# Performance work log

Hardware: AMD Instinct MI355X
Metric: run time of the kernel (lower is better)

The kernel has to match this reference:

```python
import jax, jax.numpy as jnp
import numpy as np

N = 50000      # nodes
E = 400000     # edges (before self-loops)
DIN = 128
HID = 128
HEADS = 4
DOUT = 64
NEG_SLOPE = 0.2  # PyG GATConv default


def setup_inputs() -> dict:
    key = jax.random.key(0)
    ks = jax.random.split(key, 14)

    def w(k, shape, fan_in):
        return jax.random.normal(k, shape, dtype=jnp.float32) * (1.0 / np.sqrt(fan_in))

    x = jax.random.normal(ks[0], (N, DIN), dtype=jnp.float32)
    edge_index = jax.random.randint(ks[1], (2, E), 0, N, dtype=jnp.int32)

    # layer 1: DIN -> HEADS*HID (concat)
    W1 = w(ks[2], (DIN, HEADS * HID), DIN)
    a_src1 = w(ks[3], (HEADS, HID), HID)
    a_dst1 = w(ks[4], (HEADS, HID), HID)
    b1 = jnp.zeros((HEADS * HID,), jnp.float32)
    # layer 2: HEADS*HID -> HEADS*HID (concat)
    W2 = w(ks[5], (HEADS * HID, HEADS * HID), HEADS * HID)
    a_src2 = w(ks[6], (HEADS, HID), HID)
    a_dst2 = w(ks[7], (HEADS, HID), HID)
    b2 = jnp.zeros((HEADS * HID,), jnp.float32)
    # layer 3: HEADS*HID -> DOUT, heads=1, concat=False (mean)
    W3 = w(ks[8], (HEADS * HID, DOUT), HEADS * HID)
    a_src3 = w(ks[9], (1, DOUT), DOUT)
    a_dst3 = w(ks[10], (1, DOUT), DOUT)
    b3 = jnp.zeros((DOUT,), jnp.float32)

    return dict(x=x, edge_index=edge_index,
                W1=W1, a_src1=a_src1, a_dst1=a_dst1, b1=b1,
                W2=W2, a_src2=a_src2, a_dst2=a_dst2, b2=b2,
                W3=W3, a_src3=a_src3, a_dst3=a_dst3, b3=b3)


def _gat_layer(x, src, dst, W, a_src, a_dst, n):
    """One GATConv (eval mode, self-loops already in src/dst). Returns [n, H, C]."""
    H, C = a_src.shape
    h = (x @ W).reshape(n, H, C)                        # projected features
    alpha_s = jnp.einsum('nhc,hc->nh', h, a_src)        # per-node src logits
    alpha_d = jnp.einsum('nhc,hc->nh', h, a_dst)
    e = jax.nn.leaky_relu(alpha_s[src] + alpha_d[dst], NEG_SLOPE)  # [E', H]
    # segment softmax over incoming edges of each dst node
    m = jax.ops.segment_max(e, dst, num_segments=n)
    e = jnp.exp(e - m[dst])
    s = jax.ops.segment_sum(e, dst, num_segments=n)
    alpha = e / (s[dst] + 1e-16)                        # [E', H]
    msg = h[src] * alpha[:, :, None]                    # [E', H, C]
    return jax.ops.segment_sum(msg, dst, num_segments=n)


def reference(x, edge_index, W1, a_src1, a_dst1, b1,
              W2, a_src2, a_dst2, b2, W3, a_src3, a_dst3, b3):
    n = x.shape[0]
    loops = jnp.arange(n, dtype=edge_index.dtype)       # PyG add_self_loops=True
    src = jnp.concatenate([edge_index[0], loops])
    dst = jnp.concatenate([edge_index[1], loops])

    h = _gat_layer(x, src, dst, W1, a_src1, a_dst1, n).reshape(n, -1) + b1
    h = jax.nn.elu(h)   # dropout is identity in eval mode
    h = _gat_layer(h, src, dst, W2, a_src2, a_dst2, n).reshape(n, -1) + b2
    h = jax.nn.elu(h)
    out = _gat_layer(h, src, dst, W3, a_src3, a_dst3, n)[:, 0, :] + b3  # heads=1, concat=False
    return out
```

## Files before the change

kernel.cpp:

```cpp
#include <hip/hip_runtime.h>
#include <hip/hip_bf16.h>


typedef __attribute__((ext_vector_type(8))) short bf16x8;
typedef __attribute__((ext_vector_type(4))) float f32x4;

__device__ __forceinline__ float bflo(unsigned w) { return __uint_as_float(w << 16); }
__device__ __forceinline__ float bfhi(unsigned w) { return __uint_as_float(w & 0xffff0000u); }
__device__ __forceinline__ float leaky(float x) { return x > 0.f ? x : 0.2f * x; }


__global__ void k_count(const int* __restrict__ ei, int E, int N, int* __restrict__ cnt) {
    int e = blockIdx.x * blockDim.x + threadIdx.x;
    int tot = E + N;
    if (e >= tot) return;
    int d = (e < E) ? ei[E + e] : (e - E);
    atomicAdd(&cnt[d], 1);
}

__global__ void k_scan1(const int* __restrict__ cnt, int N, int* __restrict__ rp,
                        int* __restrict__ blksum) {
    __shared__ int sdata[256];
    int t = threadIdx.x;
    int base = blockIdx.x * 1024;
    int v[4];
    int loc = 0;
#pragma unroll
    for (int i = 0; i < 4; i++) {
        int idx = base + t * 4 + i;
        v[i] = (idx < N) ? ((cnt[idx] + 3) & ~3) : 0;
        loc += v[i];
    }
    int x = loc;
    sdata[t] = x;
    __syncthreads();
    for (int off = 1; off < 256; off <<= 1) {
        int y = (t >= off) ? sdata[t - off] : 0;
        __syncthreads();
        x += y;
        sdata[t] = x;
        __syncthreads();
    }
    int run = x - loc;
#pragma unroll
    for (int i = 0; i < 4; i++) {
        int idx = base + t * 4 + i;
        if (idx < N) rp[idx] = run;
        run += v[i];
    }
    if (t == 255) blksum[blockIdx.x] = x;
}

__global__ void k_scan2(const int* __restrict__ blksum, int nblk, int* __restrict__ blkoff) {
    int l = threadIdx.x;
    int v = (l < nblk) ? blksum[l] : 0;
    int x = v;
#pragma unroll
    for (int off = 1; off < 64; off <<= 1) {
        int y = __shfl_up(x, off);
        if (l >= off) x += y;
    }
    if (l < nblk) blkoff[l] = x - v;
}

__global__ void k_scan3(int* __restrict__ rp, const int* __restrict__ blkoff,
                        const int* __restrict__ blksum, int N, int nblk,
                        int* __restrict__ cur) {
    int i = blockIdx.x * blockDim.x + threadIdx.x;
    if (i < N) {
        int v = rp[i] + blkoff[i >> 10];
        rp[i] = v;
        cur[i] = v;
    }
    if (i == 0) rp[N] = blkoff[nblk - 1] + blksum[nblk - 1];
}

__global__ void k_fill(const int* __restrict__ ei, int E, int N, int* __restrict__ cur,
                       int* __restrict__ col, int* __restrict__ dste) {
    int e = blockIdx.x * blockDim.x + threadIdx.x;
    int tot = E + N;
    if (e >= tot) return;
    int s, d;
    if (e < E) { s = ei[e]; d = ei[E + e]; }
    else       { s = e - E; d = e - E; }
    int p = atomicAdd(&cur[d], 1);
    col[p] = s;
    dste[p] = d;
}

__global__ void k_padfill(const int* __restrict__ rp, const int* __restrict__ cnt, int N,
                          int* __restrict__ col, int* __restrict__ dste) {
    int n = blockIdx.x * blockDim.x + threadIdx.x;
    if (n >= N) return;
    int p = rp[n] + cnt[n];
    int end = rp[n + 1];
    for (; p < end; p++) {
        col[p] = 0;
        dste[p] = -1;
    }
}


__global__ void k_cast_pad(const float* __restrict__ X, __hip_bfloat16* __restrict__ Xb,
                           int n_elems, int total) {
    int i = (blockIdx.x * blockDim.x + threadIdx.x) * 4;
    if (i >= total) return;
    float4 v = make_float4(0.f, 0.f, 0.f, 0.f);
    if (i < n_elems) v = *(const float4*)&X[i];
    __hip_bfloat16 tmp[4] = {__float2bfloat16(v.x), __float2bfloat16(v.y),
                             __float2bfloat16(v.z), __float2bfloat16(v.w)};
    *(ushort4*)&Xb[i] = *(const ushort4*)tmp;
}

__global__ void k_castT(const float* __restrict__ W, __hip_bfloat16* __restrict__ Wt,
                        int K, int Nw) {
    __shared__ float t[32][33];
    int k0 = blockIdx.x * 32, n0 = blockIdx.y * 32;
    int tx = threadIdx.x & 31, ty = threadIdx.x >> 5;
    for (int i = ty; i < 32; i += 8) t[i][tx] = W[(size_t)(k0 + i) * Nw + n0 + tx];
    __syncthreads();
    for (int i = ty; i < 32; i += 8)
        Wt[(size_t)(n0 + i) * K + k0 + tx] = __float2bfloat16(t[tx][i]);
}


template <int BN>
__global__ void __launch_bounds__(256) k_gemm_mfma(const __hip_bfloat16* __restrict__ A,
                                                   const __hip_bfloat16* __restrict__ Bt,
                                                   __hip_bfloat16* __restrict__ C,
                                                   int M, int Nn, int K) {
    constexpr int BM = 128, BK = 64;
    constexpr int WM = 64;
    constexpr int WN = BN / 2;
    constexpr int MREP = WM / 16;
    constexpr int NREP = WN / 16;

    __shared__ __hip_bfloat16 lds[(BM + BN) * BK];
    __hip_bfloat16* As = lds;
    __hip_bfloat16* Bs = lds + BM * BK;

    const int tid = threadIdx.x;
    const int wave = tid >> 6;
    const int lane = tid & 63;
    const int wm0 = (wave >> 1) * WM;
    const int wn0 = (wave & 1) * WN;
    const int m0 = blockIdx.y * BM;
    const int n0 = blockIdx.x * BN;
    const int fr = lane & 15;
    const int fq = lane >> 4;

    f32x4 acc[MREP][NREP] = {};

    for (int kt = 0; kt < K; kt += BK) {
        const __hip_bfloat16* srcA = A + (size_t)m0 * K + kt;
#pragma unroll
        for (int it = 0; it < BM * 8 / 256; ++it) {
            int gb = it * 256 + wave * 64;
            int g = gb + lane;
            int row = g >> 3;
            int kg = (g & 7) ^ (row & 7);
            const __hip_bfloat16* gsrc = srcA + (size_t)row * K + kg * 8;
            __builtin_amdgcn_global_load_lds(
                (const __attribute__((address_space(1))) void*)gsrc,
                (__attribute__((address_space(3))) void*)(As + gb * 8), 16, 0, 0);
        }
        const __hip_bfloat16* srcB = Bt + (size_t)n0 * K + kt;
#pragma unroll
        for (int it = 0; it < BN * 8 / 256; ++it) {
            int gb = it * 256 + wave * 64;
            int g = gb + lane;
            int row = g >> 3;
            int kg = (g & 7) ^ (row & 7);
            const __hip_bfloat16* gsrc = srcB + (size_t)row * K + kg * 8;
            __builtin_amdgcn_global_load_lds(
                (const __attribute__((address_space(1))) void*)gsrc,
                (__attribute__((address_space(3))) void*)(Bs + gb * 8), 16, 0, 0);
        }
        __syncthreads();

#pragma unroll
        for (int sl = 0; sl < 2; ++sl) {
            int ke = sl * 32 + fq * 8;
            bf16x8 af[MREP], bfr[NREP];
#pragma unroll
            for (int i = 0; i < MREP; ++i) {
                int row = wm0 + i * 16 + fr;
                int e = (row * BK + ke) ^ ((row & 7) << 3);
                af[i] = *(const bf16x8*)(As + e);
            }
#pragma unroll
            for (int j = 0; j < NREP; ++j) {
                int row = wn0 + j * 16 + fr;
                int e = (row * BK + ke) ^ ((row & 7) << 3);
                bfr[j] = *(const bf16x8*)(Bs + e);
            }
#pragma unroll
            for (int i = 0; i < MREP; ++i)
#pragma unroll
                for (int j = 0; j < NREP; ++j)
                    acc[i][j] = __builtin_amdgcn_mfma_f32_16x16x32_bf16(
                        af[i], bfr[j], acc[i][j], 0, 0, 0);
        }
        __syncthreads();
    }

#pragma unroll
    for (int i = 0; i < MREP; ++i) {
#pragma unroll
        for (int j = 0; j < NREP; ++j) {
            int col = n0 + wn0 + j * 16 + fr;
#pragma unroll
            for (int r = 0; r < 4; ++r) {
                int rowg = m0 + wm0 + i * 16 + fq * 4 + r;
                C[(size_t)rowg * Nn + col] = __float2bfloat16(acc[i][j][r]);
            }
        }
    }
}


template <int C, int H>
__global__ void k_alpha(const __hip_bfloat16* __restrict__ h, const float* __restrict__ a_src,
                        const float* __restrict__ a_dst, float* __restrict__ as_out,
                        float* __restrict__ ad_out, int N) {
    int w = (blockIdx.x * blockDim.x + threadIdx.x) >> 6;
    int lane = threadIdx.x & 63;
    int n = w / H, hd = w % H;
    if (n >= N) return;
    const __hip_bfloat16* hp = h + (size_t)n * (C * H) + hd * C;
    const float* asp = a_src + hd * C;
    const float* adp = a_dst + hd * C;
    float s1 = 0.f, s2 = 0.f;
    if constexpr (C == 128) {
        unsigned wrd = *(const unsigned*)(hp + 2 * lane);
        float f0 = bflo(wrd), f1 = bfhi(wrd);
        float2 a2 = *(const float2*)(asp + 2 * lane);
        float2 d2 = *(const float2*)(adp + 2 * lane);
        s1 = f0 * a2.x + f1 * a2.y;
        s2 = f0 * d2.x + f1 * d2.y;
    } else {
        float v = __bfloat162float(hp[lane & 63]);
        s1 = v * asp[lane];
        s2 = v * adp[lane];
    }
#pragma unroll
    for (int off = 32; off >= 1; off >>= 1) {
        s1 += __shfl_xor(s1, off);
        s2 += __shfl_xor(s2, off);
    }
    if (lane == 0) {
        as_out[n * H + hd] = s1;
        ad_out[n * H + hd] = s2;
    }
}


__global__ void k_edgew4(const int* __restrict__ col, const int* __restrict__ dste,
                         const float* __restrict__ as, const float* __restrict__ ad,
                         float* __restrict__ wbuf, const int* __restrict__ rp, int N, int EP) {
    int e = blockIdx.x * blockDim.x + threadIdx.x;
    int rpN = rp[N];
    if (e >= rpN) return;
    int d = dste[e];
    if (d < 0) {
        wbuf[e] = 0.f;
        wbuf[EP + e] = 0.f;
        wbuf[2 * EP + e] = 0.f;
        wbuf[3 * EP + e] = 0.f;
        return;
    }
    int s = col[e];
    float4 a = *(const float4*)&as[s * 4];
    float4 b = *(const float4*)&ad[d * 4];
    wbuf[e]          = __expf(leaky(a.x + b.x));
    wbuf[EP + e]     = __expf(leaky(a.y + b.y));
    wbuf[2 * EP + e] = __expf(leaky(a.z + b.z));
    wbuf[3 * EP + e] = __expf(leaky(a.w + b.w));
}

__global__ void k_edgew1(const int* __restrict__ col, const int* __restrict__ dste,
                         const float* __restrict__ as, const float* __restrict__ ad,
                         float* __restrict__ wbuf, const int* __restrict__ rp, int N) {
    int e = blockIdx.x * blockDim.x + threadIdx.x;
    int rpN = rp[N];
    if (e >= rpN) return;
    int d = dste[e];
    if (d < 0) { wbuf[e] = 0.f; return; }
    wbuf[e] = __expf(leaky(as[col[e]] + ad[d]));
}


template <bool DO_ELU>
__global__ void k_gather512(const __hip_bfloat16* __restrict__ hfeat,
                            const float* __restrict__ wbuf, const int* __restrict__ rp,
                            const int* __restrict__ col, const float* __restrict__ bias,
                            __hip_bfloat16* __restrict__ out, int N, int EP) {
    int w = (blockIdx.x * blockDim.x + threadIdx.x) >> 6;
    int lane = threadIdx.x & 63;
    if (w >= N) return;
    int d = w;
    int r0 = rp[d], r1 = rp[d + 1];
    const float* wp = wbuf + (size_t)(lane >> 4) * EP;

    float acc[8] = {};
    float wsum = 0.f;
    for (int e = r0; e < r1; e += 4) {
        int4 c4 = *(const int4*)&col[e];
        float4 w4 = *(const float4*)&wp[e];
        uint4 v0 = *(const uint4*)(hfeat + (size_t)c4.x * 512 + lane * 8);
        uint4 v1 = *(const uint4*)(hfeat + (size_t)c4.y * 512 + lane * 8);
        uint4 v2 = *(const uint4*)(hfeat + (size_t)c4.z * 512 + lane * 8);
        uint4 v3 = *(const uint4*)(hfeat + (size_t)c4.w * 512 + lane * 8);
        wsum += (w4.x + w4.y) + (w4.z + w4.w);
        acc[0] += w4.x * bflo(v0.x); acc[1] += w4.x * bfhi(v0.x);
        acc[2] += w4.x * bflo(v0.y); acc[3] += w4.x * bfhi(v0.y);
        acc[4] += w4.x * bflo(v0.z); acc[5] += w4.x * bfhi(v0.z);
        acc[6] += w4.x * bflo(v0.w); acc[7] += w4.x * bfhi(v0.w);
        acc[0] += w4.y * bflo(v1.x); acc[1] += w4.y * bfhi(v1.x);
        acc[2] += w4.y * bflo(v1.y); acc[3] += w4.y * bfhi(v1.y);
        acc[4] += w4.y * bflo(v1.z); acc[5] += w4.y * bfhi(v1.z);
        acc[6] += w4.y * bflo(v1.w); acc[7] += w4.y * bfhi(v1.w);
        acc[0] += w4.z * bflo(v2.x); acc[1] += w4.z * bfhi(v2.x);
        acc[2] += w4.z * bflo(v2.y); acc[3] += w4.z * bfhi(v2.y);
        acc[4] += w4.z * bflo(v2.z); acc[5] += w4.z * bfhi(v2.z);
        acc[6] += w4.z * bflo(v2.w); acc[7] += w4.z * bfhi(v2.w);
        acc[0] += w4.w * bflo(v3.x); acc[1] += w4.w * bfhi(v3.x);
        acc[2] += w4.w * bflo(v3.y); acc[3] += w4.w * bfhi(v3.y);
        acc[4] += w4.w * bflo(v3.z); acc[5] += w4.w * bfhi(v3.z);
        acc[6] += w4.w * bflo(v3.w); acc[7] += w4.w * bfhi(v3.w);
    }

    float inv = 1.0f / (wsum + 1e-16f);
    __hip_bfloat16 tmp[8];
#pragma unroll
    for (int j = 0; j < 8; j++) {
        float v = acc[j] * inv + bias[lane * 8 + j];
        if (DO_ELU) v = v > 0.f ? v : expm1f(v);
        tmp[j] = __float2bfloat16(v);
    }
    *(float4*)(out + (size_t)d * 512 + lane * 8) = *(const float4*)tmp;
}


__global__ void k_gather64(const __hip_bfloat16* __restrict__ hfeat,
                           const float* __restrict__ wbuf, const int* __restrict__ rp,
                           const int* __restrict__ col, const float* __restrict__ bias,
                           float* __restrict__ out, int N) {
    int w = (blockIdx.x * blockDim.x + threadIdx.x) >> 6;
    int lane = threadIdx.x & 63;
    if (w >= N) return;
    int d = w;
    int r0 = rp[d], r1 = rp[d + 1];
    int g = lane >> 4, cl = lane & 15;

    float a0 = 0.f, a1 = 0.f, a2 = 0.f, a3 = 0.f, wsum = 0.f;
    for (int e0 = r0; e0 < r1; e0 += 4) {
        int e = e0 + g;
        int s = col[e];
        float wf = wbuf[e];
        uint2 q = *(const uint2*)(hfeat + (size_t)s * 64 + cl * 4);
        wsum += wf;
        a0 += wf * bflo(q.x);
        a1 += wf * bfhi(q.x);
        a2 += wf * bflo(q.y);
        a3 += wf * bfhi(q.y);
    }
#pragma unroll
    for (int off = 16; off <= 32; off <<= 1) {
        a0 += __shfl_xor(a0, off);
        a1 += __shfl_xor(a1, off);
        a2 += __shfl_xor(a2, off);
        a3 += __shfl_xor(a3, off);
        wsum += __shfl_xor(wsum, off);
    }
    if (g == 0) {
        float inv = 1.0f / (wsum + 1e-16f);
        float4 b4 = *(const float4*)&bias[cl * 4];
        float4 o = make_float4(a0 * inv + b4.x, a1 * inv + b4.y,
                               a2 * inv + b4.z, a3 * inv + b4.w);
        *(float4*)(out + (size_t)d * 64 + cl * 4) = o;
    }
}


extern "C" void kernel_launch(void* const* d_in, const int* in_sizes, int n_in,
                              void* d_out, int out_size, void* d_ws, size_t ws_size,
                              hipStream_t stream) {
    const float* x   = (const float*)d_in[0];
    const int*   ei  = (const int*)d_in[1];
    const float* W1  = (const float*)d_in[2];
    const float* as1 = (const float*)d_in[3];
    const float* ad1 = (const float*)d_in[4];
    const float* b1  = (const float*)d_in[5];
    const float* W2  = (const float*)d_in[6];
    const float* as2 = (const float*)d_in[7];
    const float* ad2 = (const float*)d_in[8];
    const float* b2  = (const float*)d_in[9];
    const float* W3  = (const float*)d_in[10];
    const float* as3 = (const float*)d_in[11];
    const float* ad3 = (const float*)d_in[12];
    const float* b3  = (const float*)d_in[13];

    const int N = in_sizes[0] / 128;
    const int E = in_sizes[1] / 2;
    const int Etot = E + N;
    const int EP = (Etot + 3 * N + 255) & ~255;
    const int Mp = (N + 127) & ~127;

    char* ws = (char*)d_ws;
    size_t off = 0;
    auto alloc = [&](size_t bytes) -> void* {
        void* p = ws + off;
        off = (off + bytes + 255) & ~(size_t)255;
        return p;
    };
    __hip_bfloat16* hbuf = (__hip_bfloat16*)alloc((size_t)Mp * 512 * 2);
    __hip_bfloat16* fbuf = (__hip_bfloat16*)alloc((size_t)Mp * 512 * 2);
    __hip_bfloat16* xb   = (__hip_bfloat16*)alloc((size_t)Mp * 128 * 2);
    __hip_bfloat16* Wt1  = (__hip_bfloat16*)alloc((size_t)512 * 128 * 2);
    __hip_bfloat16* Wt2  = (__hip_bfloat16*)alloc((size_t)512 * 512 * 2);
    __hip_bfloat16* Wt3  = (__hip_bfloat16*)alloc((size_t)64 * 512 * 2);
    float* aS   = (float*)alloc((size_t)N * 4 * 4);
    float* aD   = (float*)alloc((size_t)N * 4 * 4);
    float* wbuf = (float*)alloc((size_t)EP * 4 * 4);
    int* cnt  = (int*)alloc((size_t)N * 4);
    int* rp   = (int*)alloc((size_t)(N + 1) * 4);
    int* cur  = (int*)alloc((size_t)N * 4);
    int* col  = (int*)alloc((size_t)EP * 4);
    int* dste = (int*)alloc((size_t)EP * 4);
    int* blks = (int*)alloc(64 * 4);
    int* blko = (int*)alloc(64 * 4);

    hipMemsetAsync(cnt, 0, (size_t)N * 4, stream);
    int thr = 256;
    k_count<<<(Etot + thr - 1) / thr, thr, 0, stream>>>(ei, E, N, cnt);
    int nblk = (N + 1023) / 1024;
    k_scan1<<<nblk, 256, 0, stream>>>(cnt, N, rp, blks);
    k_scan2<<<1, 64, 0, stream>>>(blks, nblk, blko);
    k_scan3<<<(N + 255) / 256, 256, 0, stream>>>(rp, blko, blks, N, nblk, cur);
    k_fill<<<(Etot + thr - 1) / thr, thr, 0, stream>>>(ei, E, N, cur, col, dste);
    k_padfill<<<(N + 255) / 256, 256, 0, stream>>>(rp, cnt, N, col, dste);

    {
        int total = Mp * 128;
        k_cast_pad<<<(total / 4 + 255) / 256, 256, 0, stream>>>(x, xb, N * 128, total);
        dim3 g1(128 / 32, 512 / 32);
        k_castT<<<g1, 256, 0, stream>>>(W1, Wt1, 128, 512);
        dim3 g2(512 / 32, 512 / 32);
        k_castT<<<g2, 256, 0, stream>>>(W2, Wt2, 512, 512);
        dim3 g3(512 / 32, 64 / 32);
        k_castT<<<g3, 256, 0, stream>>>(W3, Wt3, 512, 64);
    }

    int alphaBlocks4 = (int)(((size_t)N * 4 * 64 + 255) / 256);
    int alphaBlocks1 = (int)(((size_t)N * 64 + 255) / 256);
    int edgeBlocks = (EP + 255) / 256;
    int gatBlocks = (N + 3) / 4;
    dim3 gemmG(512 / 128, Mp / 128);
    dim3 gemmG3(1, Mp / 128);

    k_gemm_mfma<128><<<gemmG, 256, 0, stream>>>(xb, Wt1, hbuf, Mp, 512, 128);
    k_alpha<128, 4><<<alphaBlocks4, 256, 0, stream>>>(hbuf, as1, ad1, aS, aD, N);
    k_edgew4<<<edgeBlocks, 256, 0, stream>>>(col, dste, aS, aD, wbuf, rp, N, EP);
    k_gather512<true><<<gatBlocks, 256, 0, stream>>>(hbuf, wbuf, rp, col, b1, fbuf, N, EP);

    k_gemm_mfma<128><<<gemmG, 256, 0, stream>>>(fbuf, Wt2, hbuf, Mp, 512, 512);
    k_alpha<128, 4><<<alphaBlocks4, 256, 0, stream>>>(hbuf, as2, ad2, aS, aD, N);
    k_edgew4<<<edgeBlocks, 256, 0, stream>>>(col, dste, aS, aD, wbuf, rp, N, EP);
    k_gather512<true><<<gatBlocks, 256, 0, stream>>>(hbuf, wbuf, rp, col, b2, fbuf, N, EP);

    k_gemm_mfma<64><<<gemmG3, 256, 0, stream>>>(fbuf, Wt3, hbuf, Mp, 64, 512);
    k_alpha<64, 1><<<alphaBlocks1, 256, 0, stream>>>(hbuf, as3, ad3, aS, aD, N);
    k_edgew1<<<edgeBlocks, 256, 0, stream>>>(col, dste, aS, aD, wbuf, rp, N);
    k_gather64<<<gatBlocks, 256, 0, stream>>>(hbuf, wbuf, rp, col, b3, (float*)d_out, N);
}
```

Measured before the change: 437.6 us.

## Reorder layer-1 GAT to aggregate raw inputs before projection, fuse bias+ELU into GEMM

Layer 1 now computes attention logits directly from the bf16 inputs using the precomputed products W1·a_src and W1·a_dst. It aggregates the 128-wide inputs per head before the projection, then runs a per-head batched GEMM with bias and ELU fused into the epilogue. This replaces a 512-wide gather over projected features with a 128-wide gather per head. The layer-2 gather is split across heads via grid z, and the padding fill is folded into the scan kernel, which removes one launch. The cost is an extra aggregated buffer and a GEMM over four 128-column blocks, and the reordering changes where bf16 rounding occurs.

```diff
diff --git a/kernel.cpp b/kernel.cpp
--- a/kernel.cpp
+++ b/kernel.cpp
@@ -8,6 +8,11 @@
 __device__ __forceinline__ float bflo(unsigned w) { return __uint_as_float(w << 16); }
 __device__ __forceinline__ float bfhi(unsigned w) { return __uint_as_float(w & 0xffff0000u); }
 __device__ __forceinline__ float leaky(float x) { return x > 0.f ? x : 0.2f * x; }
+__device__ __forceinline__ unsigned pack2(float a, float b) {
+    unsigned ua = __bfloat16_as_ushort(__float2bfloat16(a));
+    unsigned ub = __bfloat16_as_ushort(__float2bfloat16(b));
+    return ua | (ub << 16);
+}
 
 
 __global__ void k_count(const int* __restrict__ ei, int E, int N, int* __restrict__ cnt) {
@@ -64,13 +69,20 @@
 }
 
 __global__ void k_scan3(int* __restrict__ rp, const int* __restrict__ blkoff,
-                        const int* __restrict__ blksum, int N, int nblk,
-                        int* __restrict__ cur) {
+                        const int* __restrict__ blksum, const int* __restrict__ cnt,
+                        int N, int nblk, int* __restrict__ cur,
+                        int* __restrict__ col, int* __restrict__ dste) {
     int i = blockIdx.x * blockDim.x + threadIdx.x;
     if (i < N) {
         int v = rp[i] + blkoff[i >> 10];
         rp[i] = v;
         cur[i] = v;
+        int c = cnt[i];
+        int pad = ((c + 3) & ~3) - c;
+        for (int p = 0; p < pad; p++) {
+            col[v + c + p] = 0;
+            dste[v + c + p] = -1;
+        }
     }
     if (i == 0) rp[N] = blkoff[nblk - 1] + blksum[nblk - 1];
 }
@@ -88,18 +100,6 @@
     dste[p] = d;
 }
 
-__global__ void k_padfill(const int* __restrict__ rp, const int* __restrict__ cnt, int N,
-                          int* __restrict__ col, int* __restrict__ dste) {
-    int n = blockIdx.x * blockDim.x + threadIdx.x;
-    if (n >= N) return;
-    int p = rp[n] + cnt[n];
-    int end = rp[n + 1];
-    for (; p < end; p++) {
-        col[p] = 0;
-        dste[p] = -1;
-    }
-}
-
 
 __global__ void k_cast_pad(const float* __restrict__ X, __hip_bfloat16* __restrict__ Xb,
                            int n_elems, int total) {
@@ -123,12 +123,63 @@
         Wt[(size_t)(n0 + i) * K + k0 + tx] = __float2bfloat16(t[tx][i]);
 }
 
-
-template <int BN>
+__global__ void k_va1(const float* __restrict__ W1, const float* __restrict__ asrc,
+                      const float* __restrict__ adst, float* __restrict__ va8) {
+    int t = threadIdx.x;
+    int c = t >> 2, h = t & 3;
+    const float* wrow = W1 + (size_t)c * 512 + h * 128;
+    const float* av = asrc + h * 128;
+    const float* dv = adst + h * 128;
+    float vs = 0.f, vd = 0.f;
+    for (int k = 0; k < 128; k++) {
+        float wv = wrow[k];
+        vs += wv * av[k];
+        vd += wv * dv[k];
+    }
+    va8[c * 8 + h] = vs;
+    va8[c * 8 + 4 + h] = vd;
+}
+
+__global__ void k_alpha_x(const __hip_bfloat16* __restrict__ xb,
+                          const float* __restrict__ va8, float* __restrict__ as_out,
+                          float* __restrict__ ad_out, int N) {
+    int w = (blockIdx.x * blockDim.x + threadIdx.x) >> 6;
+    int lane = threadIdx.x & 63;
+    if (w >= N) return;
+    unsigned wrd = ((const unsigned*)xb)[(size_t)w * 64 + lane];
+    float f0 = bflo(wrd), f1 = bfhi(wrd);
+    int c0 = lane * 2;
+    float4 vs0 = *(const float4*)&va8[c0 * 8];
+    float4 vd0 = *(const float4*)&va8[c0 * 8 + 4];
+    float4 vs1 = *(const float4*)&va8[(c0 + 1) * 8];
+    float4 vd1 = *(const float4*)&va8[(c0 + 1) * 8 + 4];
+    float s[8];
+    s[0] = f0 * vs0.x + f1 * vs1.x;
+    s[1] = f0 * vs0.y + f1 * vs1.y;
+    s[2] = f0 * vs0.z + f1 * vs1.z;
+    s[3] = f0 * vs0.w + f1 * vs1.w;
+    s[4] = f0 * vd0.x + f1 * vd1.x;
+    s[5] = f0 * vd0.y + f1 * vd1.y;
+    s[6] = f0 * vd0.z + f1 * vd1.z;
+    s[7] = f0 * vd0.w + f1 * vd1.w;
+#pragma unroll
+    for (int off = 32; off >= 1; off >>= 1)
+#pragma unroll
+        for (int j = 0; j < 8; j++) s[j] += __shfl_xor(s[j], off);
+    if (lane == 0) {
+        *(float4*)&as_out[w * 4] = make_float4(s[0], s[1], s[2], s[3]);
+        *(float4*)&ad_out[w * 4] = make_float4(s[4], s[5], s[6], s[7]);
+    }
+}
+
+
+template <int BN, bool FUSE>
 __global__ void __launch_bounds__(256) k_gemm_mfma(const __hip_bfloat16* __restrict__ A,
                                                    const __hip_bfloat16* __restrict__ Bt,
                                                    __hip_bfloat16* __restrict__ C,
-                                                   int M, int Nn, int K) {
+                                                   int lda, int ldc, int K,
+                                                   int hsA, int hsB, int hsC,
+                                                   const float* __restrict__ bias) {
     constexpr int BM = 128, BK = 64;
     constexpr int WM = 64;
     constexpr int WN = BN / 2;
@@ -138,6 +189,11 @@
     __shared__ __hip_bfloat16 lds[(BM + BN) * BK];
     __hip_bfloat16* As = lds;
     __hip_bfloat16* Bs = lds + BM * BK;
+
+    const int z = blockIdx.z;
+    A += (size_t)z * hsA;
+    Bt += (size_t)z * hsB;
+    const int cbase = z * hsC;
 
     const int tid = threadIdx.x;
     const int wave = tid >> 6;
@@ -152,14 +208,14 @@
     f32x4 acc[MREP][NREP] = {};
 
     for (int kt = 0; kt < K; kt += BK) {
-        const __hip_bfloat16* srcA = A + (size_t)m0 * K + kt;
+        const __hip_bfloat16* srcA = A + (size_t)m0 * lda + kt;
 #pragma unroll
         for (int it = 0; it < BM * 8 / 256; ++it) {
             int gb = it * 256 + wave * 64;
             int g = gb + lane;
             int row = g >> 3;
             int kg = (g & 7) ^ (row & 7);
-            const __hip_bfloat16* gsrc = srcA + (size_t)row * K + kg * 8;
+            const __hip_bfloat16* gsrc = srcA + (size_t)row * lda + kg * 8;
             __builtin_amdgcn_global_load_lds(
                 (const __attribute__((address_space(1))) void*)gsrc,
                 (__attribute__((address_space(3))) void*)(As + gb * 8), 16, 0, 0);
@@ -208,11 +264,16 @@
     for (int i = 0; i < MREP; ++i) {
 #pragma unroll
         for (int j = 0; j < NREP; ++j) {
-            int col = n0 + wn0 + j * 16 + fr;
+            int colg = cbase + n0 + wn0 + j * 16 + fr;
 #pragma unroll
             for (int r = 0; r < 4; ++r) {
                 int rowg = m0 + wm0 + i * 16 + fq * 4 + r;
-                C[(size_t)rowg * Nn + col] = __float2bfloat16(acc[i][j][r]);
+                float v = acc[i][j][r];
+                if (FUSE) {
+                    v += bias[colg];
+                    v = v > 0.f ? v : expm1f(v);
+                }
+                C[(size_t)rowg * ldc + colg] = __float2bfloat16(v);
             }
         }
     }
@@ -255,90 +316,151 @@
 }
 
 
-__global__ void k_edgew4(const int* __restrict__ col, const int* __restrict__ dste,
+__global__ void k_edgewA(const int* __restrict__ col, const int* __restrict__ dste,
                          const float* __restrict__ as, const float* __restrict__ ad,
-                         float* __restrict__ wbuf, const int* __restrict__ rp, int N, int EP) {
+                         float* __restrict__ wA, const int* __restrict__ rp, int N) {
     int e = blockIdx.x * blockDim.x + threadIdx.x;
-    int rpN = rp[N];
-    if (e >= rpN) return;
+    if (e >= rp[N]) return;
     int d = dste[e];
     if (d < 0) {
-        wbuf[e] = 0.f;
-        wbuf[EP + e] = 0.f;
-        wbuf[2 * EP + e] = 0.f;
-        wbuf[3 * EP + e] = 0.f;
+        *(float4*)&wA[e * 4] = make_float4(0.f, 0.f, 0.f, 0.f);
         return;
     }
     int s = col[e];
     float4 a = *(const float4*)&as[s * 4];
     float4 b = *(const float4*)&ad[d * 4];
-    wbuf[e]          = __expf(leaky(a.x + b.x));
-    wbuf[EP + e]     = __expf(leaky(a.y + b.y));
-    wbuf[2 * EP + e] = __expf(leaky(a.z + b.z));
-    wbuf[3 * EP + e] = __expf(leaky(a.w + b.w));
+    float4 w;
+    w.x = __expf(leaky(a.x + b.x));
+    w.y = __expf(leaky(a.y + b.y));
+    w.z = __expf(leaky(a.z + b.z));
+    w.w = __expf(leaky(a.w + b.w));
+    *(float4*)&wA[e * 4] = w;
+}
+
+
+__global__ void k_edgewS(const int* __restrict__ col, const int* __restrict__ dste,
+                         const float* __restrict__ as, const float* __restrict__ ad,
+                         float* __restrict__ wS, const int* __restrict__ rp, int N, int EP) {
+    int e = blockIdx.x * blockDim.x + threadIdx.x;
+    if (e >= rp[N]) return;
+    int d = dste[e];
+    if (d < 0) {
+        wS[e] = 0.f; wS[EP + e] = 0.f; wS[2 * EP + e] = 0.f; wS[3 * EP + e] = 0.f;
+        return;
+    }
+    int s = col[e];
+    float4 a = *(const float4*)&as[s * 4];
+    float4 b = *(const float4*)&ad[d * 4];
+    wS[e]          = __expf(leaky(a.x + b.x));
+    wS[EP + e]     = __expf(leaky(a.y + b.y));
+    wS[2 * EP + e] = __expf(leaky(a.z + b.z));
+    wS[3 * EP + e] = __expf(leaky(a.w + b.w));
 }
 
 __global__ void k_edgew1(const int* __restrict__ col, const int* __restrict__ dste,
                          const float* __restrict__ as, const float* __restrict__ ad,
-                         float* __restrict__ wbuf, const int* __restrict__ rp, int N) {
+                         float* __restrict__ wS, const int* __restrict__ rp, int N) {
     int e = blockIdx.x * blockDim.x + threadIdx.x;
-    int rpN = rp[N];
-    if (e >= rpN) return;
+    if (e >= rp[N]) return;
     int d = dste[e];
-    if (d < 0) { wbuf[e] = 0.f; return; }
-    wbuf[e] = __expf(leaky(as[col[e]] + ad[d]));
-}
-
-
-template <bool DO_ELU>
-__global__ void k_gather512(const __hip_bfloat16* __restrict__ hfeat,
-                            const float* __restrict__ wbuf, const int* __restrict__ rp,
-                            const int* __restrict__ col, const float* __restrict__ bias,
-                            __hip_bfloat16* __restrict__ out, int N, int EP) {
+    if (d < 0) { wS[e] = 0.f; return; }
+    wS[e] = __expf(leaky(as[col[e]] + ad[d]));
+}
+
+
+__global__ void k_gatherX(const __hip_bfloat16* __restrict__ xb,
+                          const float* __restrict__ wA, const int* __restrict__ rp,
+                          const int* __restrict__ col, unsigned* __restrict__ out32, int N) {
     int w = (blockIdx.x * blockDim.x + threadIdx.x) >> 6;
     int lane = threadIdx.x & 63;
     if (w >= N) return;
     int d = w;
     int r0 = rp[d], r1 = rp[d + 1];
-    const float* wp = wbuf + (size_t)(lane >> 4) * EP;
+    const unsigned* xp = (const unsigned*)xb;
 
     float acc[8] = {};
-    float wsum = 0.f;
+    float ws0 = 0.f, ws1 = 0.f, ws2 = 0.f, ws3 = 0.f;
+    for (int e = r0; e < r1; e += 4) {
+        int4 c4 = *(const int4*)&col[e];
+        float4 w0 = *(const float4*)&wA[e * 4];
+        float4 w1 = *(const float4*)&wA[e * 4 + 4];
+        float4 w2 = *(const float4*)&wA[e * 4 + 8];
+        float4 w3 = *(const float4*)&wA[e * 4 + 12];
+        unsigned v0 = xp[(size_t)c4.x * 64 + lane];
+        unsigned v1 = xp[(size_t)c4.y * 64 + lane];
+        unsigned v2 = xp[(size_t)c4.z * 64 + lane];
+        unsigned v3 = xp[(size_t)c4.w * 64 + lane];
+        ws0 += w0.x + w1.x + w2.x + w3.x;
+        ws1 += w0.y + w1.y + w2.y + w3.y;
+        ws2 += w0.z + w1.z + w2.z + w3.z;
+        ws3 += w0.w + w1.w + w2.w + w3.w;
+        float f0, f1;
+        f0 = bflo(v0); f1 = bfhi(v0);
+        acc[0] += w0.x * f0; acc[1] += w0.x * f1;
+        acc[2] += w0.y * f0; acc[3] += w0.y * f1;
+        acc[4] += w0.z * f0; acc[5] += w0.z * f1;
+        acc[6] += w0.w * f0; acc[7] += w0.w * f1;
+        f0 = bflo(v1); f1 = bfhi(v1);
+        acc[0] += w1.x * f0; acc[1] += w1.x * f1;
+        acc[2] += w1.y * f0; acc[3] += w1.y * f1;
+        acc[4] += w1.z * f0; acc[5] += w1.z * f1;
+        acc[6] += w1.w * f0; acc[7] += w1.w * f1;
+        f0 = bflo(v2); f1 = bfhi(v2);
+        acc[0] += w2.x * f0; acc[1] += w2.x * f1;
+        acc[2] += w2.y * f0; acc[3] += w2.y * f1;
+        acc[4] += w2.z * f0; acc[5] += w2.z * f1;
+        acc[6] += w2.w * f0; acc[7] += w2.w * f1;
+        f0 = bflo(v3); f1 = bfhi(v3);
+        acc[0] += w3.x * f0; acc[1] += w3.x * f1;
+        acc[2] += w3.y * f0; acc[3] += w3.y * f1;
+        acc[4] += w3.z * f0; acc[5] += w3.z * f1;
+        acc[6] += w3.w * f0; acc[7] += w3.w * f1;
+    }
+    float i0 = 1.f / (ws0 + 1e-16f), i1 = 1.f / (ws1 + 1e-16f);
+    float i2 = 1.f / (ws2 + 1e-16f), i3 = 1.f / (ws3 + 1e-16f);
+    size_t ob = (size_t)d * 256 + lane;
+    out32[ob]       = pack2(acc[0] * i0, acc[1] * i0);
+    out32[ob + 64]  = pack2(acc[2] * i1, acc[3] * i1);
+    out32[ob + 128] = pack2(acc[4] * i2, acc[5] * i2);
+    out32[ob + 192] = pack2(acc[6] * i3, acc[7] * i3);
+}
+
+
+__global__ void k_gatherH(const __hip_bfloat16* __restrict__ hfeat,
+                          const float* __restrict__ wS, const int* __restrict__ rp,
+                          const int* __restrict__ col, const float* __restrict__ bias,
+                          unsigned* __restrict__ out32, int N, int EP) {
+    int w = (blockIdx.x * blockDim.x + threadIdx.x) >> 6;
+    int lane = threadIdx.x & 63;
+    if (w >= N) return;
+    int hd = blockIdx.z;
+    int d = w;
+    int r0 = rp[d], r1 = rp[d + 1];
+    const float* wp = wS + (size_t)hd * EP;
+    const unsigned* hp = (const unsigned*)hfeat;
+    const int coff = hd * 64 + lane;
+
+    float a0 = 0.f, a1 = 0.f, wsum = 0.f;
     for (int e = r0; e < r1; e += 4) {
         int4 c4 = *(const int4*)&col[e];
         float4 w4 = *(const float4*)&wp[e];
-        uint4 v0 = *(const uint4*)(hfeat + (size_t)c4.x * 512 + lane * 8);
-        uint4 v1 = *(const uint4*)(hfeat + (size_t)c4.y * 512 + lane * 8);
-        uint4 v2 = *(const uint4*)(hfeat + (size_t)c4.z * 512 + lane * 8);
-        uint4 v3 = *(const uint4*)(hfeat + (size_t)c4.w * 512 + lane * 8);
+        unsigned v0 = hp[(size_t)c4.x * 256 + coff];
+        unsigned v1 = hp[(size_t)c4.y * 256 + coff];
+        unsigned v2 = hp[(size_t)c4.z * 256 + coff];
+        unsigned v3 = hp[(size_t)c4.w * 256 + coff];
         wsum += (w4.x + w4.y) + (w4.z + w4.w);
-        acc[0] += w4.x * bflo(v0.x); acc[1] += w4.x * bfhi(v0.x);
-        acc[2] += w4.x * bflo(v0.y); acc[3] += w4.x * bfhi(v0.y);
-        acc[4] += w4.x * bflo(v0.z); acc[5] += w4.x * bfhi(v0.z);
-        acc[6] += w4.x * bflo(v0.w); acc[7] += w4.x * bfhi(v0.w);
-        acc[0] += w4.y * bflo(v1.x); acc[1] += w4.y * bfhi(v1.x);
-        acc[2] += w4.y * bflo(v1.y); acc[3] += w4.y * bfhi(v1.y);
-        acc[4] += w4.y * bflo(v1.z); acc[5] += w4.y * bfhi(v1.z);
-        acc[6] += w4.y * bflo(v1.w); acc[7] += w4.y * bfhi(v1.w);
-        acc[0] += w4.z * bflo(v2.x); acc[1] += w4.z * bfhi(v2.x);
-        acc[2] += w4.z * bflo(v2.y); acc[3] += w4.z * bfhi(v2.y);
-        acc[4] += w4.z * bflo(v2.z); acc[5] += w4.z * bfhi(v2.z);
-        acc[6] += w4.z * bflo(v2.w); acc[7] += w4.z * bfhi(v2.w);
-        acc[0] += w4.w * bflo(v3.x); acc[1] += w4.w * bfhi(v3.x);
-        acc[2] += w4.w * bflo(v3.y); acc[3] += w4.w * bfhi(v3.y);
-        acc[4] += w4.w * bflo(v3.z); acc[5] += w4.w * bfhi(v3.z);
-        acc[6] += w4.w * bflo(v3.w); acc[7] += w4.w * bfhi(v3.w);
-    }
-
-    float inv = 1.0f / (wsum + 1e-16f);
-    __hip_bfloat16 tmp[8];
-#pragma unroll
-    for (int j = 0; j < 8; j++) {
-        float v = acc[j] * inv + bias[lane * 8 + j];
-        if (DO_ELU) v = v > 0.f ? v : expm1f(v);
-        tmp[j] = __float2bfloat16(v);
-    }
-    *(float4*)(out + (size_t)d * 512 + lane * 8) = *(const float4*)tmp;
+        a0 += w4.x * bflo(v0); a1 += w4.x * bfhi(v0);
+        a0 += w4.y * bflo(v1); a1 += w4.y * bfhi(v1);
+        a0 += w4.z * bflo(v2); a1 += w4.z * bfhi(v2);
+        a0 += w4.w * bflo(v3); a1 += w4.w * bfhi(v3);
+    }
+    float inv = 1.f / (wsum + 1e-16f);
+    int c = hd * 128 + lane * 2;
+    float o0 = a0 * inv + bias[c];
+    float o1 = a1 * inv + bias[c + 1];
+    o0 = o0 > 0.f ? o0 : expm1f(o0);
+    o1 = o1 > 0.f ? o1 : expm1f(o1);
+    out32[(size_t)d * 256 + coff] = pack2(o0, o1);
 }
 
 
@@ -416,6 +538,7 @@
     };
     __hip_bfloat16* hbuf = (__hip_bfloat16*)alloc((size_t)Mp * 512 * 2);
     __hip_bfloat16* fbuf = (__hip_bfloat16*)alloc((size_t)Mp * 512 * 2);
+    __hip_bfloat16* xagg = (__hip_bfloat16*)alloc((size_t)Mp * 512 * 2);
     __hip_bfloat16* xb   = (__hip_bfloat16*)alloc((size_t)Mp * 128 * 2);
     __hip_bfloat16* Wt1  = (__hip_bfloat16*)alloc((size_t)512 * 128 * 2);
     __hip_bfloat16* Wt2  = (__hip_bfloat16*)alloc((size_t)512 * 512 * 2);
@@ -423,6 +546,7 @@
     float* aS   = (float*)alloc((size_t)N * 4 * 4);
     float* aD   = (float*)alloc((size_t)N * 4 * 4);
     float* wbuf = (float*)alloc((size_t)EP * 4 * 4);
+    float* va8  = (float*)alloc(128 * 8 * 4);
     int* cnt  = (int*)alloc((size_t)N * 4);
     int* rp   = (int*)alloc((size_t)(N + 1) * 4);
     int* cur  = (int*)alloc((size_t)N * 4);
@@ -437,9 +561,8 @@
     int nblk = (N + 1023) / 1024;
     k_scan1<<<nblk, 256, 0, stream>>>(cnt, N, rp, blks);
     k_scan2<<<1, 64, 0, stream>>>(blks, nblk, blko);
-    k_scan3<<<(N + 255) / 256, 256, 0, stream>>>(rp, blko, blks, N, nblk, cur);
+    k_scan3<<<(N + 255) / 256, 256, 0, stream>>>(rp, blko, blks, cnt, N, nblk, cur, col, dste);
     k_fill<<<(Etot + thr - 1) / thr, thr, 0, stream>>>(ei, E, N, cur, col, dste);
-    k_padfill<<<(N + 255) / 256, 256, 0, stream>>>(rp, cnt, N, col, dste);
 
     {
         int total = Mp * 128;
@@ -450,26 +573,41 @@
         k_castT<<<g2, 256, 0, stream>>>(W2, Wt2, 512, 512);
         dim3 g3(512 / 32, 64 / 32);
         k_castT<<<g3, 256, 0, stream>>>(W3, Wt3, 512, 64);
+        k_va1<<<1, 512, 0, stream>>>(W1, as1, ad1, va8);
     }
 
     int alphaBlocks4 = (int)(((size_t)N * 4 * 64 + 255) / 256);
     int alphaBlocks1 = (int)(((size_t)N * 64 + 255) / 256);
     int edgeBlocks = (EP + 255) / 256;
     int gatBlocks = (N + 3) / 4;
-    dim3 gemmG(512 / 128, Mp / 128);
-    dim3 gemmG3(1, Mp / 128);
-
-    k_gemm_mfma<128><<<gemmG, 256, 0, stream>>>(xb, Wt1, hbuf, Mp, 512, 128);
-    k_alpha<128, 4><<<alphaBlocks4, 256, 0, stream>>>(hbuf, as1, ad1, aS, aD, N);
-    k_edgew4<<<edgeBlocks, 256, 0, stream>>>(col, dste, aS, aD, wbuf, rp, N, EP);
-    k_gather512<true><<<gatBlocks, 256, 0, stream>>>(hbuf, wbuf, rp, col, b1, fbuf, N, EP);
-
-    k_gemm_mfma<128><<<gemmG, 256, 0, stream>>>(fbuf, Wt2, hbuf, Mp, 512, 512);
+
+    k_alpha_x<<<gatBlocks, 256, 0, stream>>>(xb, va8, aS, aD, N);
+    k_edgewA<<<edgeBlocks, 256, 0, stream>>>(col, dste, aS, aD, wbuf, rp, N);
+    k_gatherX<<<gatBlocks, 256, 0, stream>>>(xb, wbuf, rp, col, (unsigned*)xagg, N);
+    {
+        dim3 g(1, Mp / 128, 4);
+        k_gemm_mfma<128, true><<<g, 256, 0, stream>>>(xagg, Wt1, fbuf,
+                                                      512, 512, 128,
+                                                      128, 128 * 128, 128, b1);
+    }
+
+    {
+        dim3 g(4, Mp / 128, 1);
+        k_gemm_mfma<128, false><<<g, 256, 0, stream>>>(fbuf, Wt2, hbuf,
+                                                       512, 512, 512, 0, 0, 0, nullptr);
+    }
     k_alpha<128, 4><<<alphaBlocks4, 256, 0, stream>>>(hbuf, as2, ad2, aS, aD, N);
-    k_edgew4<<<edgeBlocks, 256, 0, stream>>>(col, dste, aS, aD, wbuf, rp, N, EP);
-    k_gather512<true><<<gatBlocks, 256, 0, stream>>>(hbuf, wbuf, rp, col, b2, fbuf, N, EP);
-
-    k_gemm_mfma<64><<<gemmG3, 256, 0, stream>>>(fbuf, Wt3, hbuf, Mp, 64, 512);
+    k_edgewS<<<edgeBlocks, 256, 0, stream>>>(col, dste, aS, aD, wbuf, rp, N, EP);
+    {
+        dim3 g(gatBlocks, 1, 4);
+        k_gatherH<<<g, 256, 0, stream>>>(hbuf, wbuf, rp, col, b2, (unsigned*)fbuf, N, EP);
+    }
+
+    {
+        dim3 g(1, Mp / 128, 1);
+        k_gemm_mfma<64, false><<<g, 256, 0, stream>>>(fbuf, Wt3, hbuf,
+                                                      512, 64, 512, 0, 0, 0, nullptr);
+    }
     k_alpha<64, 1><<<alphaBlocks1, 256, 0, stream>>>(hbuf, as3, ad3, aS, aD, N);
     k_edgew1<<<edgeBlocks, 256, 0, stream>>>(col, dste, aS, aD, wbuf, rp, N);
     k_gather64<<<gatBlocks, 256, 0, stream>>>(hbuf, wbuf, rp, col, b3, (float*)d_out, N);
```

New measurement: 417.8 us. -4.5%, faster.
